# Kernel optimization log

Hardware: AMD Instinct MI355X
Metric: run time of the kernel (lower is better)

The kernel has to match this reference:

```python
import jax, jax.numpy as jnp
import numpy as np

B, S, H, F, E, K = 4, 2048, 2048, 8192, 8, 2  # batch, seq, hidden, d_ff, num_experts, topk


def setup_inputs() -> dict:
    key = jax.random.key(0)
    k0, k1, k2, k3 = jax.random.split(key, 4)
    x = jax.random.normal(k0, (B, S, H), dtype=jnp.float32)
    Wr = jax.random.normal(k1, (H, E), dtype=jnp.float32) * 0.02   # router weight
    br = jnp.zeros((E,), dtype=jnp.float32)
    W1 = jax.random.normal(k2, (E, H, F), dtype=jnp.float32) * 0.02  # per-expert up-proj
    b1 = jnp.zeros((E, F), dtype=jnp.float32)
    W2 = jax.random.normal(k3, (E, F, H), dtype=jnp.float32) * 0.02  # per-expert down-proj
    b2 = jnp.zeros((E, H), dtype=jnp.float32)
    return {"x": x, "Wr": Wr, "br": br, "W1": W1, "b1": b1, "W2": W2, "b2": b2}


def reference(x, Wr, br, W1, b1, W2, b2):
    b, s, h = x.shape
    xt = x.reshape(b * s, h)                      # (N, H), N = b*s
    logits = xt @ Wr + br                         # (N, E) router
    gates = jax.nn.softmax(logits, axis=-1)
    G, idx = jax.lax.top_k(gates, K)              # (N, K), (N, K)
    P = jax.nn.one_hot(idx, E, dtype=xt.dtype)    # (N, K, E) dispatch one-hot
    # tokens_for_expert: einsum('nk,nh->kh', P[...,e], x) for each expert -> (E, K, H)
    tok = jnp.einsum('nke,nh->ekh', P, xt)
    # per-expert FFN (exact GELU, matching torch nn.GELU default)
    mid = jax.nn.gelu(jnp.einsum('ekh,ehf->ekf', tok, W1) + b1[:, None, :], approximate=False)
    Eo = jnp.einsum('ekf,efh->ekh', mid, W2) + b2[:, None, :]   # (E, K, H)
    # combine: sum_e einsum('nk,kh->nh', G, E_e)
    y = jnp.einsum('nk,ekh->nh', G, Eo)
    return y.reshape(b, s, h)
```

## Files before the change

kernel.cpp:

```cpp
#include <hip/hip_runtime.h>
#include <math.h>

#define NTOK 8192
#define HDIM 2048
#define FDIM 8192
#define NEXP 8

typedef float f32x4 __attribute__((ext_vector_type(4)));

__global__ __launch_bounds__(256) void router_kernel(const float* __restrict__ x,
                                                     const float* __restrict__ Wr,
                                                     const float* __restrict__ br,
                                                     const float* __restrict__ b2,
                                                     float* __restrict__ G,
                                                     int* __restrict__ sel,
                                                     float* __restrict__ tok,
                                                     float* __restrict__ ebar) {
  {
    const int idx = blockIdx.x * 256 + threadIdx.x;
    if (idx < (16 * HDIM) / 4) {
      *(float4*)(tok + idx * 4) = make_float4(0.f, 0.f, 0.f, 0.f);
    } else if (idx < (16 * HDIM) / 4 + 1024) {
      const int j = idx - (16 * HDIM) / 4;
      const int h = (j & 511) << 2;
      float4 s = make_float4(0.f, 0.f, 0.f, 0.f);
#pragma unroll
      for (int e = 0; e < 8; ++e) {
        float4 b = *(const float4*)(b2 + e * HDIM + h);
        s.x += b.x; s.y += b.y; s.z += b.z; s.w += b.w;
      }
      *(float4*)(ebar + (j >> 9) * HDIM + h) = s;
    }
  }
  const int wave = threadIdx.x >> 6;
  const int lane = threadIdx.x & 63;
  const int n0 = (blockIdx.x * 4 + wave) * 4;

  float acc[4][8];
#pragma unroll
  for (int t = 0; t < 4; ++t)
#pragma unroll
    for (int e = 0; e < 8; ++e) acc[t][e] = 0.f;

#pragma unroll 4
  for (int j = 0; j < 32; ++j) {
    const int h = lane + (j << 6);
    float4 wa = *(const float4*)(Wr + h * 8);
    float4 wb = *(const float4*)(Wr + h * 8 + 4);
    float w[8] = {wa.x, wa.y, wa.z, wa.w, wb.x, wb.y, wb.z, wb.w};
#pragma unroll
    for (int t = 0; t < 4; ++t) {
      float xv = x[(size_t)(n0 + t) * HDIM + h];
#pragma unroll
      for (int e = 0; e < 8; ++e) acc[t][e] = fmaf(xv, w[e], acc[t][e]);
    }
  }

#pragma unroll
  for (int t = 0; t < 4; ++t)
#pragma unroll
    for (int e = 0; e < 8; ++e) {
      float v = acc[t][e];
      v += __shfl_xor(v, 1, 64);
      v += __shfl_xor(v, 2, 64);
      v += __shfl_xor(v, 4, 64);
      v += __shfl_xor(v, 8, 64);
      v += __shfl_xor(v, 16, 64);
      v += __shfl_xor(v, 32, 64);
      acc[t][e] = v;
    }

  if (lane == 0) {
    float brv[8];
#pragma unroll
    for (int e = 0; e < 8; ++e) brv[e] = br[e];
#pragma unroll
    for (int t = 0; t < 4; ++t) {
      float l[8];
#pragma unroll
      for (int e = 0; e < 8; ++e) l[e] = acc[t][e] + brv[e];
      float m = l[0];
#pragma unroll
      for (int e = 1; e < 8; ++e) m = fmaxf(m, l[e]);
      float s = 0.f;
#pragma unroll
      for (int e = 0; e < 8; ++e) s += expf(l[e] - m);
      float best = l[0], second = -3.4e38f;
      int bi = 0, si = 0;
#pragma unroll
      for (int e = 1; e < 8; ++e) {
        float v = l[e];
        if (v > best) { second = best; si = bi; best = v; bi = e; }
        else if (v > second) { second = v; si = e; }
      }
      const int n = n0 + t;
      const float inv = 1.f / s;
      G[n * 2 + 0] = expf(best - m) * inv;
      G[n * 2 + 1] = expf(second - m) * inv;
      sel[n * 2 + 0] = bi;
      sel[n * 2 + 1] = si;
    }
  }
}

__global__ __launch_bounds__(256) void tok_kernel(const float* __restrict__ x,
                                                  const int* __restrict__ sel,
                                                  float* __restrict__ tok) {
  __shared__ float2 part[16][256];
  __shared__ int sidx[256];
  const int tid = threadIdx.x;
  const int h0 = blockIdx.x << 9;
  const int n0 = blockIdx.y << 7;
#pragma unroll
  for (int s = 0; s < 16; ++s) part[s][tid] = make_float2(0.f, 0.f);
  sidx[tid] = sel[(n0 << 1) + tid];
  __syncthreads();
#pragma unroll 8
  for (int i = 0; i < 128; ++i) {
    float2 v = *(const float2*)(x + (size_t)(n0 + i) * HDIM + h0 + tid * 2);
    int s0 = sidx[2 * i] << 1;
    int s1 = (sidx[2 * i + 1] << 1) + 1;
    part[s0][tid].x += v.x; part[s0][tid].y += v.y;
    part[s1][tid].x += v.x; part[s1][tid].y += v.y;
  }
#pragma unroll
  for (int s = 0; s < 16; ++s) {
    atomicAdd(&tok[s * HDIM + h0 + tid * 2 + 0], part[s][tid].x);
    atomicAdd(&tok[s * HDIM + h0 + tid * 2 + 1], part[s][tid].y);
  }
}

__global__ __launch_bounds__(256) void up_kernel(const float* __restrict__ tok,
                                                 const float* __restrict__ W1,
                                                 float* __restrict__ up_part) {
  const int e = blockIdx.z;
  const int hc = blockIdx.y;
  const int tid = threadIdx.x;
  const int f = (blockIdx.x << 10) + (tid << 2);
  const int h0 = hc << 7;
  __shared__ float t0s[128], t1s[128];
  if (tid < 128) t0s[tid] = tok[(e * 2 + 0) * HDIM + h0 + tid];
  else           t1s[tid - 128] = tok[(e * 2 + 1) * HDIM + h0 + (tid - 128)];
  __syncthreads();
  const float* Wp = W1 + ((size_t)e * HDIM + h0) * FDIM + f;
  float4 a0 = make_float4(0.f, 0.f, 0.f, 0.f), a1 = make_float4(0.f, 0.f, 0.f, 0.f);
#pragma unroll 16
  for (int hh = 0; hh < 128; ++hh) {
    f32x4 w = __builtin_nontemporal_load(reinterpret_cast<const f32x4*>(Wp + (size_t)hh * FDIM));
    float t0 = t0s[hh], t1 = t1s[hh];
    a0.x = fmaf(t0, w.x, a0.x); a0.y = fmaf(t0, w.y, a0.y);
    a0.z = fmaf(t0, w.z, a0.z); a0.w = fmaf(t0, w.w, a0.w);
    a1.x = fmaf(t1, w.x, a1.x); a1.y = fmaf(t1, w.y, a1.y);
    a1.z = fmaf(t1, w.z, a1.z); a1.w = fmaf(t1, w.w, a1.w);
  }
  float* p0 = up_part + ((size_t)((e * 16 + hc) * 2 + 0) * FDIM) + f;
  float* p1 = up_part + ((size_t)((e * 16 + hc) * 2 + 1) * FDIM) + f;
  *(float4*)p0 = a0;
  *(float4*)p1 = a1;
}

__global__ __launch_bounds__(256) void down_kernel(const float* __restrict__ up_part,
                                                   const float* __restrict__ b1,
                                                   const float* __restrict__ W2,
                                                   float* __restrict__ down_part) {
  const int e = blockIdx.z;
  const int fc = blockIdx.x;
  const int tid = threadIdx.x;
  const int f0 = fc << 7;
  const int h = (blockIdx.y << 10) + (tid << 2);
  __shared__ float ms[2][128];
  {
    const int k = tid >> 7;
    const int fl = tid & 127;
    float acc = 0.f;
#pragma unroll
    for (int hc = 0; hc < 16; ++hc)
      acc += up_part[(size_t)((e * 16 + hc) * 2 + k) * FDIM + f0 + fl];
    acc += b1[e * FDIM + f0 + fl];
    ms[k][fl] = 0.5f * acc * (1.f + erff(acc * 0.70710678118654752f));
  }
  __syncthreads();
  const float* Wp = W2 + ((size_t)e * FDIM + f0) * HDIM + h;
  float4 a0 = make_float4(0.f, 0.f, 0.f, 0.f), a1 = make_float4(0.f, 0.f, 0.f, 0.f);
#pragma unroll 16
  for (int ff = 0; ff < 128; ++ff) {
    f32x4 w = __builtin_nontemporal_load(reinterpret_cast<const f32x4*>(Wp + (size_t)ff * HDIM));
    float m0 = ms[0][ff], m1 = ms[1][ff];
    a0.x = fmaf(m0, w.x, a0.x); a0.y = fmaf(m0, w.y, a0.y);
    a0.z = fmaf(m0, w.z, a0.z); a0.w = fmaf(m0, w.w, a0.w);
    a1.x = fmaf(m1, w.x, a1.x); a1.y = fmaf(m1, w.y, a1.y);
    a1.z = fmaf(m1, w.z, a1.z); a1.w = fmaf(m1, w.w, a1.w);
  }
  float* p0 = down_part + ((size_t)((e * 64 + fc) * 2 + 0) * HDIM) + h;
  float* p1 = down_part + ((size_t)((e * 64 + fc) * 2 + 1) * HDIM) + h;
  *(float4*)p0 = a0;
  *(float4*)p1 = a1;
}

__global__ __launch_bounds__(256) void ebar_reduce_kernel(const float* __restrict__ down_part,
                                                          float* __restrict__ ebar) {
  const int tid = threadIdx.x;
  const int c0 = blockIdx.x * 8;
  float4 acc[2][2];
#pragma unroll
  for (int k = 0; k < 2; ++k)
#pragma unroll
    for (int r = 0; r < 2; ++r) acc[k][r] = make_float4(0.f, 0.f, 0.f, 0.f);
#pragma unroll
  for (int j = 0; j < 8; ++j) {
    const int c = c0 + j;
#pragma unroll
    for (int k = 0; k < 2; ++k) {
      const float* base = down_part + (size_t)(c * 2 + k) * HDIM;
#pragma unroll
      for (int r = 0; r < 2; ++r) {
        float4 v = *(const float4*)(base + ((r << 8) + tid) * 4);
        acc[k][r].x += v.x; acc[k][r].y += v.y; acc[k][r].z += v.z; acc[k][r].w += v.w;
      }
    }
  }
#pragma unroll
  for (int k = 0; k < 2; ++k)
#pragma unroll
    for (int r = 0; r < 2; ++r) {
      float* dst = ebar + k * HDIM + ((r << 8) + tid) * 4;
      atomicAdd(dst + 0, acc[k][r].x);
      atomicAdd(dst + 1, acc[k][r].y);
      atomicAdd(dst + 2, acc[k][r].z);
      atomicAdd(dst + 3, acc[k][r].w);
    }
}

__global__ __launch_bounds__(256) void combine_kernel(const float* __restrict__ G,
                                                      const float* __restrict__ ebar,
                                                      float* __restrict__ y) {
  const int i4 = blockIdx.x * 256 + threadIdx.x;
  const int n = i4 >> 9;
  const int h = (i4 & 511) << 2;
  const float g0 = G[n * 2 + 0], g1 = G[n * 2 + 1];
  float4 e0 = *(const float4*)(ebar + h);
  float4 e1 = *(const float4*)(ebar + HDIM + h);
  f32x4 r;
  r.x = fmaf(g0, e0.x, g1 * e1.x);
  r.y = fmaf(g0, e0.y, g1 * e1.y);
  r.z = fmaf(g0, e0.z, g1 * e1.z);
  r.w = fmaf(g0, e0.w, g1 * e1.w);
  __builtin_nontemporal_store(r, reinterpret_cast<f32x4*>(y + ((size_t)n << 11) + h));
}

extern "C" void kernel_launch(void* const* d_in, const int* in_sizes, int n_in,
                              void* d_out, int out_size, void* d_ws, size_t ws_size,
                              hipStream_t stream) {
  const float* x  = (const float*)d_in[0];
  const float* Wr = (const float*)d_in[1];
  const float* br = (const float*)d_in[2];
  const float* W1 = (const float*)d_in[3];
  const float* b1 = (const float*)d_in[4];
  const float* W2 = (const float*)d_in[5];
  const float* b2 = (const float*)d_in[6];
  float* y = (float*)d_out;

  char* ws = (char*)d_ws;
  float* G         = (float*)(ws);
  int*   sel       = (int*)(ws + (64 << 10));
  float* tok       = (float*)(ws + (128 << 10));
  float* ebar      = (float*)(ws + (256 << 10));
  float* up_part   = (float*)(ws + (512 << 10));
  float* down_part = (float*)(ws + (512 << 10) + (8 << 20));

  router_kernel<<<512, 256, 0, stream>>>(x, Wr, br, b2, G, sel, tok, ebar);
  tok_kernel<<<dim3(4, 64), 256, 0, stream>>>(x, sel, tok);
  up_kernel<<<dim3(8, 16, 8), 256, 0, stream>>>(tok, W1, up_part);
  down_kernel<<<dim3(64, 2, 8), 256, 0, stream>>>(up_part, b1, W2, down_part);
  ebar_reduce_kernel<<<64, 256, 0, stream>>>(down_part, ebar);
  combine_kernel<<<16384, 256, 0, stream>>>(G, ebar, y);
}
```

Before: 262.2 us.

## Retile up/down GEMV kernels so each block streams full contiguous weight rows

The up-projection now uses one block per 32-row H chunk per expert, and each thread reads 8 float4 columns across the full F row. The down-projection now uses one block per 128-row F chunk covering the full H row. The aim is longer contiguous weight streams per block and fewer blocks. The trade-offs are more split-K partials (64 instead of 16) that the down kernel must sum, a larger up_part workspace, and fewer blocks in flight for down (512 vs 1024). Register pressure also rises in up_kernel.

New measurement: 258.7 us. About the same (-1.3%).

```diff
diff --git a/kernel.cpp b/kernel.cpp
--- a/kernel.cpp
+++ b/kernel.cpp
@@ -133,68 +133,92 @@
 __global__ __launch_bounds__(256) void up_kernel(const float* __restrict__ tok,
                                                  const float* __restrict__ W1,
                                                  float* __restrict__ up_part) {
-  const int e = blockIdx.z;
-  const int hc = blockIdx.y;
+  const int e = blockIdx.y;
+  const int hc = blockIdx.x;
   const int tid = threadIdx.x;
-  const int f = (blockIdx.x << 10) + (tid << 2);
-  const int h0 = hc << 7;
-  __shared__ float t0s[128], t1s[128];
-  if (tid < 128) t0s[tid] = tok[(e * 2 + 0) * HDIM + h0 + tid];
-  else           t1s[tid - 128] = tok[(e * 2 + 1) * HDIM + h0 + (tid - 128)];
+  const int h0 = hc << 5;
+  __shared__ float ts[2][32];
+  if (tid < 32)       ts[0][tid] = tok[(e * 2 + 0) * HDIM + h0 + tid];
+  else if (tid < 64)  ts[1][tid - 32] = tok[(e * 2 + 1) * HDIM + h0 + (tid - 32)];
   __syncthreads();
-  const float* Wp = W1 + ((size_t)e * HDIM + h0) * FDIM + f;
-  float4 a0 = make_float4(0.f, 0.f, 0.f, 0.f), a1 = make_float4(0.f, 0.f, 0.f, 0.f);
-#pragma unroll 16
-  for (int hh = 0; hh < 128; ++hh) {
-    f32x4 w = __builtin_nontemporal_load(reinterpret_cast<const f32x4*>(Wp + (size_t)hh * FDIM));
-    float t0 = t0s[hh], t1 = t1s[hh];
-    a0.x = fmaf(t0, w.x, a0.x); a0.y = fmaf(t0, w.y, a0.y);
-    a0.z = fmaf(t0, w.z, a0.z); a0.w = fmaf(t0, w.w, a0.w);
-    a1.x = fmaf(t1, w.x, a1.x); a1.y = fmaf(t1, w.y, a1.y);
-    a1.z = fmaf(t1, w.z, a1.z); a1.w = fmaf(t1, w.w, a1.w);
-  }
-  float* p0 = up_part + ((size_t)((e * 16 + hc) * 2 + 0) * FDIM) + f;
-  float* p1 = up_part + ((size_t)((e * 16 + hc) * 2 + 1) * FDIM) + f;
-  *(float4*)p0 = a0;
-  *(float4*)p1 = a1;
+
+  float4 a0[8], a1[8];
+#pragma unroll
+  for (int j = 0; j < 8; ++j) {
+    a0[j] = make_float4(0.f, 0.f, 0.f, 0.f);
+    a1[j] = make_float4(0.f, 0.f, 0.f, 0.f);
+  }
+  const float* base = W1 + ((size_t)e * HDIM + h0) * FDIM;
+#pragma unroll 2
+  for (int h = 0; h < 32; ++h) {
+    const float* row = base + (size_t)h * FDIM;
+    const float t0 = ts[0][h], t1 = ts[1][h];
+#pragma unroll
+    for (int j = 0; j < 8; ++j) {
+      f32x4 w = __builtin_nontemporal_load(
+          reinterpret_cast<const f32x4*>(row + ((j << 8) + tid) * 4));
+      a0[j].x = fmaf(t0, w.x, a0[j].x); a0[j].y = fmaf(t0, w.y, a0[j].y);
+      a0[j].z = fmaf(t0, w.z, a0[j].z); a0[j].w = fmaf(t0, w.w, a0[j].w);
+      a1[j].x = fmaf(t1, w.x, a1[j].x); a1[j].y = fmaf(t1, w.y, a1[j].y);
+      a1[j].z = fmaf(t1, w.z, a1[j].z); a1[j].w = fmaf(t1, w.w, a1[j].w);
+    }
+  }
+  float* p0 = up_part + (size_t)((e * 64 + hc) * 2 + 0) * FDIM;
+  float* p1 = up_part + (size_t)((e * 64 + hc) * 2 + 1) * FDIM;
+#pragma unroll
+  for (int j = 0; j < 8; ++j) {
+    *(float4*)(p0 + ((j << 8) + tid) * 4) = a0[j];
+    *(float4*)(p1 + ((j << 8) + tid) * 4) = a1[j];
+  }
 }
 
 __global__ __launch_bounds__(256) void down_kernel(const float* __restrict__ up_part,
                                                    const float* __restrict__ b1,
                                                    const float* __restrict__ W2,
                                                    float* __restrict__ down_part) {
-  const int e = blockIdx.z;
+  const int e = blockIdx.y;
   const int fc = blockIdx.x;
   const int tid = threadIdx.x;
   const int f0 = fc << 7;
-  const int h = (blockIdx.y << 10) + (tid << 2);
   __shared__ float ms[2][128];
   {
     const int k = tid >> 7;
     const int fl = tid & 127;
     float acc = 0.f;
 #pragma unroll
-    for (int hc = 0; hc < 16; ++hc)
-      acc += up_part[(size_t)((e * 16 + hc) * 2 + k) * FDIM + f0 + fl];
+    for (int hc = 0; hc < 64; ++hc)
+      acc += up_part[(size_t)((e * 64 + hc) * 2 + k) * FDIM + f0 + fl];
     acc += b1[e * FDIM + f0 + fl];
     ms[k][fl] = 0.5f * acc * (1.f + erff(acc * 0.70710678118654752f));
   }
   __syncthreads();
-  const float* Wp = W2 + ((size_t)e * FDIM + f0) * HDIM + h;
-  float4 a0 = make_float4(0.f, 0.f, 0.f, 0.f), a1 = make_float4(0.f, 0.f, 0.f, 0.f);
-#pragma unroll 16
+
+  float4 a[2][2];
+#pragma unroll
+  for (int k = 0; k < 2; ++k)
+#pragma unroll
+    for (int j = 0; j < 2; ++j) a[k][j] = make_float4(0.f, 0.f, 0.f, 0.f);
+  const float* base = W2 + ((size_t)e * FDIM + f0) * HDIM;
+#pragma unroll 8
   for (int ff = 0; ff < 128; ++ff) {
-    f32x4 w = __builtin_nontemporal_load(reinterpret_cast<const f32x4*>(Wp + (size_t)ff * HDIM));
-    float m0 = ms[0][ff], m1 = ms[1][ff];
-    a0.x = fmaf(m0, w.x, a0.x); a0.y = fmaf(m0, w.y, a0.y);
-    a0.z = fmaf(m0, w.z, a0.z); a0.w = fmaf(m0, w.w, a0.w);
-    a1.x = fmaf(m1, w.x, a1.x); a1.y = fmaf(m1, w.y, a1.y);
-    a1.z = fmaf(m1, w.z, a1.z); a1.w = fmaf(m1, w.w, a1.w);
-  }
-  float* p0 = down_part + ((size_t)((e * 64 + fc) * 2 + 0) * HDIM) + h;
-  float* p1 = down_part + ((size_t)((e * 64 + fc) * 2 + 1) * HDIM) + h;
-  *(float4*)p0 = a0;
-  *(float4*)p1 = a1;
+    const float* row = base + (size_t)ff * HDIM;
+    const float m0 = ms[0][ff], m1 = ms[1][ff];
+#pragma unroll
+    for (int j = 0; j < 2; ++j) {
+      f32x4 w = __builtin_nontemporal_load(
+          reinterpret_cast<const f32x4*>(row + ((j << 8) + tid) * 4));
+      a[0][j].x = fmaf(m0, w.x, a[0][j].x); a[0][j].y = fmaf(m0, w.y, a[0][j].y);
+      a[0][j].z = fmaf(m0, w.z, a[0][j].z); a[0][j].w = fmaf(m0, w.w, a[0][j].w);
+      a[1][j].x = fmaf(m1, w.x, a[1][j].x); a[1][j].y = fmaf(m1, w.y, a[1][j].y);
+      a[1][j].z = fmaf(m1, w.z, a[1][j].z); a[1][j].w = fmaf(m1, w.w, a[1][j].w);
+    }
+  }
+#pragma unroll
+  for (int k = 0; k < 2; ++k) {
+    float* p = down_part + (size_t)((e * 64 + fc) * 2 + k) * HDIM;
+#pragma unroll
+    for (int j = 0; j < 2; ++j) *(float4*)(p + ((j << 8) + tid) * 4) = a[k][j];
+  }
 }
 
 __global__ __launch_bounds__(256) void ebar_reduce_kernel(const float* __restrict__ down_part,
@@ -266,12 +290,12 @@
   float* tok       = (float*)(ws + (128 << 10));
   float* ebar      = (float*)(ws + (256 << 10));
   float* up_part   = (float*)(ws + (512 << 10));
-  float* down_part = (float*)(ws + (512 << 10) + (8 << 20));
+  float* down_part = (float*)(ws + (512 << 10) + (32 << 20));
 
   router_kernel<<<512, 256, 0, stream>>>(x, Wr, br, b2, G, sel, tok, ebar);
   tok_kernel<<<dim3(4, 64), 256, 0, stream>>>(x, sel, tok);
-  up_kernel<<<dim3(8, 16, 8), 256, 0, stream>>>(tok, W1, up_part);
-  down_kernel<<<dim3(64, 2, 8), 256, 0, stream>>>(up_part, b1, W2, down_part);
+  up_kernel<<<dim3(64, 8), 256, 0, stream>>>(tok, W1, up_part);
+  down_kernel<<<dim3(64, 8), 256, 0, stream>>>(up_part, b1, W2, down_part);
   ebar_reduce_kernel<<<64, 256, 0, stream>>>(down_part, ebar);
   combine_kernel<<<16384, 256, 0, stream>>>(G, ebar, y);
 }
```

## Fuse expert up and down projections into one FFN kernel per F-slice

Applied to the files above, without the earlier changes.

Merges up_kernel and down_kernel into a single ffn_kernel. Each block owns a 256-wide F slice of one expert: it computes the full H reduction for that slice, applies bias and GELU in shared memory, then multiplies by the matching W2 rows. This drops the up_part partial-sum buffer and one launch. The tok kernel also changes to scalar loads over a narrower H tile with twice as many blocks. The cost is only 256 blocks for streaming all of W1 and W2, which may underfill the GPU and lower achievable memory bandwidth.

Measured after the change: 229.7 us, median of 2. 1.14x faster.

```diff
diff --git a/kernel.cpp b/kernel.cpp
--- a/kernel.cpp
+++ b/kernel.cpp
@@ -7,6 +7,10 @@
 #define NEXP 8
 
 typedef float f32x4 __attribute__((ext_vector_type(4)));
+
+__device__ __forceinline__ f32x4 nt_load4(const float* p) {
+  return __builtin_nontemporal_load(reinterpret_cast<const f32x4*>(p));
+}
 
 __global__ __launch_bounds__(256) void router_kernel(const float* __restrict__ x,
                                                      const float* __restrict__ Wr,
@@ -106,108 +110,111 @@
 __global__ __launch_bounds__(256) void tok_kernel(const float* __restrict__ x,
                                                   const int* __restrict__ sel,
                                                   float* __restrict__ tok) {
-  __shared__ float2 part[16][256];
+  __shared__ float part[16][256];
   __shared__ int sidx[256];
   const int tid = threadIdx.x;
-  const int h0 = blockIdx.x << 9;
+  const int h0 = blockIdx.x << 8;
   const int n0 = blockIdx.y << 7;
 #pragma unroll
-  for (int s = 0; s < 16; ++s) part[s][tid] = make_float2(0.f, 0.f);
+  for (int s = 0; s < 16; ++s) part[s][tid] = 0.f;
   sidx[tid] = sel[(n0 << 1) + tid];
   __syncthreads();
 #pragma unroll 8
   for (int i = 0; i < 128; ++i) {
-    float2 v = *(const float2*)(x + (size_t)(n0 + i) * HDIM + h0 + tid * 2);
+    float v = x[(size_t)(n0 + i) * HDIM + h0 + tid];
     int s0 = sidx[2 * i] << 1;
     int s1 = (sidx[2 * i + 1] << 1) + 1;
-    part[s0][tid].x += v.x; part[s0][tid].y += v.y;
-    part[s1][tid].x += v.x; part[s1][tid].y += v.y;
-  }
-#pragma unroll
-  for (int s = 0; s < 16; ++s) {
-    atomicAdd(&tok[s * HDIM + h0 + tid * 2 + 0], part[s][tid].x);
-    atomicAdd(&tok[s * HDIM + h0 + tid * 2 + 1], part[s][tid].y);
-  }
-}
-
-__global__ __launch_bounds__(256) void up_kernel(const float* __restrict__ tok,
-                                                 const float* __restrict__ W1,
-                                                 float* __restrict__ up_part) {
-  const int e = blockIdx.z;
-  const int hc = blockIdx.y;
+    part[s0][tid] += v;
+    part[s1][tid] += v;
+  }
+#pragma unroll
+  for (int s = 0; s < 16; ++s) atomicAdd(&tok[s * HDIM + h0 + tid], part[s][tid]);
+}
+
+__global__ __launch_bounds__(256) void ffn_kernel(const float* __restrict__ tok,
+                                                  const float* __restrict__ W1,
+                                                  const float* __restrict__ b1,
+                                                  const float* __restrict__ W2,
+                                                  float* __restrict__ down_part) {
+  const int e = blockIdx.y;
+  const int sl = blockIdx.x;
   const int tid = threadIdx.x;
-  const int f = (blockIdx.x << 10) + (tid << 2);
-  const int h0 = hc << 7;
-  __shared__ float t0s[128], t1s[128];
-  if (tid < 128) t0s[tid] = tok[(e * 2 + 0) * HDIM + h0 + tid];
-  else           t1s[tid - 128] = tok[(e * 2 + 1) * HDIM + h0 + (tid - 128)];
-  __syncthreads();
-  const float* Wp = W1 + ((size_t)e * HDIM + h0) * FDIM + f;
-  float4 a0 = make_float4(0.f, 0.f, 0.f, 0.f), a1 = make_float4(0.f, 0.f, 0.f, 0.f);
-#pragma unroll 16
-  for (int hh = 0; hh < 128; ++hh) {
-    f32x4 w = __builtin_nontemporal_load(reinterpret_cast<const f32x4*>(Wp + (size_t)hh * FDIM));
-    float t0 = t0s[hh], t1 = t1s[hh];
-    a0.x = fmaf(t0, w.x, a0.x); a0.y = fmaf(t0, w.y, a0.y);
-    a0.z = fmaf(t0, w.z, a0.z); a0.w = fmaf(t0, w.w, a0.w);
-    a1.x = fmaf(t1, w.x, a1.x); a1.y = fmaf(t1, w.y, a1.y);
-    a1.z = fmaf(t1, w.z, a1.z); a1.w = fmaf(t1, w.w, a1.w);
-  }
-  float* p0 = up_part + ((size_t)((e * 16 + hc) * 2 + 0) * FDIM) + f;
-  float* p1 = up_part + ((size_t)((e * 16 + hc) * 2 + 1) * FDIM) + f;
-  *(float4*)p0 = a0;
-  *(float4*)p1 = a1;
-}
-
-__global__ __launch_bounds__(256) void down_kernel(const float* __restrict__ up_part,
-                                                   const float* __restrict__ b1,
-                                                   const float* __restrict__ W2,
-                                                   float* __restrict__ down_part) {
-  const int e = blockIdx.z;
-  const int fc = blockIdx.x;
-  const int tid = threadIdx.x;
-  const int f0 = fc << 7;
-  const int h = (blockIdx.y << 10) + (tid << 2);
-  __shared__ float ms[2][128];
+  const int f0 = sl << 8;
+
+  __shared__ f32x4 tok_s[1024];
+  __shared__ f32x4 red[2][4][64];
+  __shared__ f32x4 ms4[2][64];
+
   {
-    const int k = tid >> 7;
-    const int fl = tid & 127;
-    float acc = 0.f;
-#pragma unroll
-    for (int hc = 0; hc < 16; ++hc)
-      acc += up_part[(size_t)((e * 16 + hc) * 2 + k) * FDIM + f0 + fl];
-    acc += b1[e * FDIM + f0 + fl];
-    ms[k][fl] = 0.5f * acc * (1.f + erff(acc * 0.70710678118654752f));
-  }
-  __syncthreads();
-  const float* Wp = W2 + ((size_t)e * FDIM + f0) * HDIM + h;
-  float4 a0 = make_float4(0.f, 0.f, 0.f, 0.f), a1 = make_float4(0.f, 0.f, 0.f, 0.f);
-#pragma unroll 16
-  for (int ff = 0; ff < 128; ++ff) {
-    f32x4 w = __builtin_nontemporal_load(reinterpret_cast<const f32x4*>(Wp + (size_t)ff * HDIM));
-    float m0 = ms[0][ff], m1 = ms[1][ff];
-    a0.x = fmaf(m0, w.x, a0.x); a0.y = fmaf(m0, w.y, a0.y);
-    a0.z = fmaf(m0, w.z, a0.z); a0.w = fmaf(m0, w.w, a0.w);
-    a1.x = fmaf(m1, w.x, a1.x); a1.y = fmaf(m1, w.y, a1.y);
-    a1.z = fmaf(m1, w.z, a1.z); a1.w = fmaf(m1, w.w, a1.w);
-  }
-  float* p0 = down_part + ((size_t)((e * 64 + fc) * 2 + 0) * HDIM) + h;
-  float* p1 = down_part + ((size_t)((e * 64 + fc) * 2 + 1) * HDIM) + h;
-  *(float4*)p0 = a0;
-  *(float4*)p1 = a1;
+    const f32x4* src = reinterpret_cast<const f32x4*>(tok + (size_t)(e * 2) * HDIM);
+#pragma unroll
+    for (int j = 0; j < 4; ++j) tok_s[j * 256 + tid] = src[j * 256 + tid];
+  }
+  __syncthreads();
+  const float* tok_f = reinterpret_cast<const float*>(tok_s);
+
+  const int fq = tid & 63;
+  const int hq = tid >> 6;
+  f32x4 a0 = {0.f, 0.f, 0.f, 0.f}, a1 = {0.f, 0.f, 0.f, 0.f};
+  const float* base1 = W1 + (size_t)e * HDIM * FDIM + f0 + (fq << 2);
+#pragma unroll 8
+  for (int i = 0; i < 512; ++i) {
+    const int h = hq + (i << 2);
+    f32x4 w = nt_load4(base1 + (size_t)h * FDIM);
+    const float t0 = tok_f[h];
+    const float t1 = tok_f[2048 + h];
+    a0 += t0 * w;
+    a1 += t1 * w;
+  }
+  red[0][hq][fq] = a0;
+  red[1][hq][fq] = a1;
+  __syncthreads();
+  if (tid < 128) {
+    const int k = tid >> 6, f = tid & 63;
+    f32x4 s = red[k][0][f] + red[k][1][f] + red[k][2][f] + red[k][3][f];
+    s += *reinterpret_cast<const f32x4*>(b1 + e * FDIM + f0 + (f << 2));
+    f32x4 r;
+    r.x = 0.5f * s.x * (1.f + erff(s.x * 0.70710678118654752f));
+    r.y = 0.5f * s.y * (1.f + erff(s.y * 0.70710678118654752f));
+    r.z = 0.5f * s.z * (1.f + erff(s.z * 0.70710678118654752f));
+    r.w = 0.5f * s.w * (1.f + erff(s.w * 0.70710678118654752f));
+    ms4[k][f] = r;
+  }
+  __syncthreads();
+  const float* ms = reinterpret_cast<const float*>(ms4);
+
+  f32x4 c00 = {0.f, 0.f, 0.f, 0.f}, c01 = {0.f, 0.f, 0.f, 0.f};
+  f32x4 c10 = {0.f, 0.f, 0.f, 0.f}, c11 = {0.f, 0.f, 0.f, 0.f};
+  const float* base2 = W2 + (size_t)(e * FDIM + f0) * HDIM + (tid << 2);
+#pragma unroll 8
+  for (int ff = 0; ff < 256; ++ff) {
+    const float* row = base2 + (size_t)ff * HDIM;
+    const float m0 = ms[ff];
+    const float m1 = ms[256 + ff];
+    f32x4 w0 = nt_load4(row);
+    f32x4 w1 = nt_load4(row + 1024);
+    c00 += m0 * w0; c01 += m0 * w1;
+    c10 += m1 * w0; c11 += m1 * w1;
+  }
+  float* p0 = down_part + (size_t)((e * 32 + sl) * 2 + 0) * HDIM + (tid << 2);
+  float* p1 = down_part + (size_t)((e * 32 + sl) * 2 + 1) * HDIM + (tid << 2);
+  *reinterpret_cast<f32x4*>(p0) = c00;
+  *reinterpret_cast<f32x4*>(p0 + 1024) = c01;
+  *reinterpret_cast<f32x4*>(p1) = c10;
+  *reinterpret_cast<f32x4*>(p1 + 1024) = c11;
 }
 
 __global__ __launch_bounds__(256) void ebar_reduce_kernel(const float* __restrict__ down_part,
                                                           float* __restrict__ ebar) {
   const int tid = threadIdx.x;
-  const int c0 = blockIdx.x * 8;
+  const int c0 = blockIdx.x * 4;
   float4 acc[2][2];
 #pragma unroll
   for (int k = 0; k < 2; ++k)
 #pragma unroll
     for (int r = 0; r < 2; ++r) acc[k][r] = make_float4(0.f, 0.f, 0.f, 0.f);
 #pragma unroll
-  for (int j = 0; j < 8; ++j) {
+  for (int j = 0; j < 4; ++j) {
     const int c = c0 + j;
 #pragma unroll
     for (int k = 0; k < 2; ++k) {
@@ -265,13 +272,11 @@
   int*   sel       = (int*)(ws + (64 << 10));
   float* tok       = (float*)(ws + (128 << 10));
   float* ebar      = (float*)(ws + (256 << 10));
-  float* up_part   = (float*)(ws + (512 << 10));
-  float* down_part = (float*)(ws + (512 << 10) + (8 << 20));
+  float* down_part = (float*)(ws + (512 << 10));
 
   router_kernel<<<512, 256, 0, stream>>>(x, Wr, br, b2, G, sel, tok, ebar);
-  tok_kernel<<<dim3(4, 64), 256, 0, stream>>>(x, sel, tok);
-  up_kernel<<<dim3(8, 16, 8), 256, 0, stream>>>(tok, W1, up_part);
-  down_kernel<<<dim3(64, 2, 8), 256, 0, stream>>>(up_part, b1, W2, down_part);
+  tok_kernel<<<dim3(8, 64), 256, 0, stream>>>(x, sel, tok);
+  ffn_kernel<<<dim3(32, 8), 256, 0, stream>>>(tok, W1, b1, W2, down_part);
   ebar_reduce_kernel<<<64, 256, 0, stream>>>(down_part, ebar);
   combine_kernel<<<16384, 256, 0, stream>>>(G, ebar, y);
 }
```
